# Kernel optimization log

Measured on AMD Instinct MI355X. Metric: run time of the kernel, lower is better.

## Reference

```python
import jax, jax.numpy as jnp
import numpy as np

D_MODEL = 1024
N_HEADS = 16
D_K = D_MODEL // N_HEADS
D_FF = 4096
B, S = 4, 2048
EPS = 1e-5


def setup_inputs() -> dict:
    key = jax.random.key(0)
    ks = jax.random.split(key, 16)
    s = 0.02
    inp = {
        'x': jax.random.normal(ks[0], (B, S, D_MODEL), dtype=jnp.float32),
        'Wq': jax.random.normal(ks[1], (D_MODEL, D_MODEL), dtype=jnp.float32) * s,
        'bq': jnp.zeros((D_MODEL,), jnp.float32),
        'Wk': jax.random.normal(ks[2], (D_MODEL, D_MODEL), dtype=jnp.float32) * s,
        'bk': jnp.zeros((D_MODEL,), jnp.float32),
        'Wv': jax.random.normal(ks[3], (D_MODEL, D_MODEL), dtype=jnp.float32) * s,
        'bv': jnp.zeros((D_MODEL,), jnp.float32),
        'Wo': jax.random.normal(ks[4], (D_MODEL, D_MODEL), dtype=jnp.float32) * s,
        'bo': jnp.zeros((D_MODEL,), jnp.float32),
        'W1': jax.random.normal(ks[5], (D_MODEL, D_FF), dtype=jnp.float32) * s,
        'b1': jnp.zeros((D_FF,), jnp.float32),
        'W2': jax.random.normal(ks[6], (D_FF, D_MODEL), dtype=jnp.float32) * s,
        'b2': jnp.zeros((D_MODEL,), jnp.float32),
        'g1': jnp.ones((D_MODEL,), jnp.float32),
        'be1': jnp.zeros((D_MODEL,), jnp.float32),
        'g2': jnp.ones((D_MODEL,), jnp.float32),
        'be2': jnp.zeros((D_MODEL,), jnp.float32),
    }
    return inp


def _layernorm(x, g, b):
    mu = jnp.mean(x, axis=-1, keepdims=True)
    var = jnp.var(x, axis=-1, keepdims=True)
    return (x - mu) * jax.lax.rsqrt(var + EPS) * g + b


def reference(x, Wq, bq, Wk, bk, Wv, bv, Wo, bo, W1, b1, W2, b2, g1, be1, g2, be2):
    # Multi-head self-attention (mask=None, dropout in eval -> identity)
    q = (x @ Wq + bq).reshape(B, S, N_HEADS, D_K).transpose(0, 2, 1, 3)  # [B,H,S,Dk]
    k = (x @ Wk + bk).reshape(B, S, N_HEADS, D_K).transpose(0, 2, 1, 3)
    v = (x @ Wv + bv).reshape(B, S, N_HEADS, D_K).transpose(0, 2, 1, 3)
    scores = jnp.einsum('bhqd,bhkd->bhqk', q, k) / jnp.sqrt(jnp.float32(D_K))
    attn = jax.nn.softmax(scores, axis=-1)
    out = jnp.einsum('bhqk,bhkd->bhqd', attn, v)          # [B,H,S,Dk]
    out = out.transpose(0, 2, 1, 3).reshape(B, S, D_MODEL)
    att_out = out @ Wo + bo
    x2 = _layernorm(x + att_out, g1, be1)
    ff = jax.nn.relu(x2 @ W1 + b1) @ W2 + b2
    return _layernorm(x2 + ff, g2, be2)
```

## Files before the change

kernel.cpp:

```cpp
#include <hip/hip_runtime.h>
#include <hip/hip_bf16.h>

typedef __attribute__((ext_vector_type(8)))  __bf16 bf16x8;
typedef __attribute__((ext_vector_type(4)))  float  f32x4;
typedef __attribute__((ext_vector_type(16))) float  f32x16;

static __device__ __forceinline__ unsigned short f2bf(float x) {
    unsigned int u = __float_as_uint(x);
    unsigned int r = (u + 0x7FFFu + ((u >> 16) & 1u)) >> 16;
    return (unsigned short)r;
}
static __device__ __forceinline__ float bf2f(unsigned short u) {
    return __uint_as_float(((unsigned int)u) << 16);
}

static __device__ __forceinline__ float fast_exp2(float x) {
    float r;
    asm volatile("v_exp_f32 %0, %1\n\ts_nop 1" : "=v"(r) : "v"(x));
    return r;
}
static __device__ __forceinline__ unsigned int cvt_pk_bf16(float a, float b) {
    unsigned int r;
    asm("v_cvt_pk_bf16_f32 %0, %1, %2" : "=v"(r) : "v"(a), "v"(b));
    return r;
}

static __device__ __forceinline__ void gload_lds16(const ushort* g, ushort* l) {
    __builtin_amdgcn_global_load_lds((const __attribute__((address_space(1))) void*)g,
                                     (__attribute__((address_space(3))) void*)l, 16, 0, 0);
}

static __device__ __forceinline__ int xcd_swz(int id, int nwg) {
    return (id & 7) * (nwg >> 3) + (id >> 3);
}

__global__ __launch_bounds__(256) void cast_bf16_kernel(const float* __restrict__ in,
                                                        ushort* __restrict__ out, int n4) {
    int i = blockIdx.x * 256 + threadIdx.x;
    if (i < n4) {
        float4 v = reinterpret_cast<const float4*>(in)[i];
        ushort4 o;
        o.x = f2bf(v.x); o.y = f2bf(v.y); o.z = f2bf(v.z); o.w = f2bf(v.w);
        reinterpret_cast<ushort4*>(out)[i] = o;
    }
}

__global__ __launch_bounds__(256) void transpose_cast_kernel(const float* __restrict__ in,
                                                             ushort* __restrict__ out,
                                                             int K, int N) {
    __shared__ float tile[32][33];
    const int tx = threadIdx.x;
    const int ty = threadIdx.y;
    const int n0 = blockIdx.x * 32;
    const int k0 = blockIdx.y * 32;
    for (int i = ty; i < 32; i += 8)
        tile[i][tx] = in[(size_t)(k0 + i) * N + n0 + tx];
    __syncthreads();
    for (int i = ty; i < 32; i += 8)
        out[(size_t)(n0 + i) * K + k0 + tx] = f2bf(tile[tx][i]);
}

template<int RELU, int OUTBF>
__global__ __launch_bounds__(256) void gemm_bt(const ushort* __restrict__ A,
                                               const ushort* __restrict__ Bt,
                                               const float* __restrict__ bias,
                                               void* __restrict__ Cp,
                                               int M, int N, int K) {
    __shared__ ushort As[128 * 32];
    __shared__ ushort Bs[128 * 32];
    const int tid  = threadIdx.x;
    const int lane = tid & 63;
    const int w    = tid >> 6;
    const int wr   = w >> 1, wc = w & 1;
    const int nwg = gridDim.x * gridDim.y;
    int wid = xcd_swz(blockIdx.y * gridDim.x + blockIdx.x, nwg);
    const int bx = wid % gridDim.x;
    const int by = wid / gridDim.x;
    const int m0 = by * 128;
    const int n0 = bx * 128;
    const int lr = lane & 15;
    const int lk = (lane >> 4) * 8;

    const int r0 = w * 32 + (lane >> 2);
    const int c8 = (lane & 3) * 8;
    const ushort* gA0 = A  + (size_t)(m0 + r0)      * K + c8;
    const ushort* gA1 = A  + (size_t)(m0 + r0 + 16) * K + c8;
    const ushort* gB0 = Bt + (size_t)(n0 + r0)      * K + c8;
    const ushort* gB1 = Bt + (size_t)(n0 + r0 + 16) * K + c8;
    ushort* lA0 = &As[w * 1024];
    ushort* lA1 = &As[w * 1024 + 512];
    ushort* lB0 = &Bs[w * 1024];
    ushort* lB1 = &Bs[w * 1024 + 512];

    f32x4 acc[4][4];
    const f32x4 z = {0.f, 0.f, 0.f, 0.f};
    for (int i = 0; i < 4; i++) for (int j = 0; j < 4; j++) acc[i][j] = z;

    for (int k0 = 0; k0 < K; k0 += 32) {
        __syncthreads();
        gload_lds16(gA0 + k0, lA0);
        gload_lds16(gA1 + k0, lA1);
        gload_lds16(gB0 + k0, lB0);
        gload_lds16(gB1 + k0, lB1);
        __syncthreads();

        bf16x8 af[4], bfr[4];
        for (int i = 0; i < 4; i++)
            af[i] = *reinterpret_cast<const bf16x8*>(&As[(wr * 64 + i * 16 + lr) * 32 + lk]);
        for (int j = 0; j < 4; j++)
            bfr[j] = *reinterpret_cast<const bf16x8*>(&Bs[(wc * 64 + j * 16 + lr) * 32 + lk]);
        for (int i = 0; i < 4; i++)
            for (int j = 0; j < 4; j++)
                acc[i][j] = __builtin_amdgcn_mfma_f32_16x16x32_bf16(af[i], bfr[j], acc[i][j], 0, 0, 0);
    }

    const int rbase = (lane >> 4) * 4;
    for (int i = 0; i < 4; i++) {
        for (int j = 0; j < 4; j++) {
            const int col = n0 + wc * 64 + j * 16 + lr;
            const float bv = bias[col];
            for (int r = 0; r < 4; r++) {
                const int row = m0 + wr * 64 + i * 16 + rbase + r;
                float v = acc[i][j][r] + bv;
                if (RELU) v = v > 0.f ? v : 0.f;
                if (OUTBF) ((ushort*)Cp)[(size_t)row * N + col] = f2bf(v);
                else       ((float*)Cp)[(size_t)row * N + col] = v;
            }
        }
    }
}

__global__ __launch_bounds__(256) void gemm_qkv(const ushort* __restrict__ A,
                                                const ushort* __restrict__ Bt,
                                                const float* __restrict__ bq,
                                                const float* __restrict__ bk,
                                                const float* __restrict__ bv,
                                                ushort* __restrict__ Cp) {
    const int K = 1024;
    __shared__ ushort As[128 * 32];
    __shared__ ushort Bs[128 * 32];
    const int tid  = threadIdx.x;
    const int lane = tid & 63;
    const int w    = tid >> 6;
    const int wr   = w >> 1, wc = w & 1;
    const int nwg = gridDim.x * gridDim.y;
    int wid = xcd_swz(blockIdx.y * gridDim.x + blockIdx.x, nwg);
    const int bx = wid % gridDim.x;
    const int by = wid / gridDim.x;
    const int m0 = by * 128;
    const int n0 = bx * 128;
    const int lr = lane & 15;
    const int lk = (lane >> 4) * 8;

    const int r0 = w * 32 + (lane >> 2);
    const int c8 = (lane & 3) * 8;
    const ushort* gA0 = A  + (size_t)(m0 + r0)      * K + c8;
    const ushort* gA1 = A  + (size_t)(m0 + r0 + 16) * K + c8;
    const ushort* gB0 = Bt + (size_t)(n0 + r0)      * K + c8;
    const ushort* gB1 = Bt + (size_t)(n0 + r0 + 16) * K + c8;
    ushort* lA0 = &As[w * 1024];
    ushort* lA1 = &As[w * 1024 + 512];
    ushort* lB0 = &Bs[w * 1024];
    ushort* lB1 = &Bs[w * 1024 + 512];

    f32x4 acc[4][4];
    const f32x4 z = {0.f, 0.f, 0.f, 0.f};
    for (int i = 0; i < 4; i++) for (int j = 0; j < 4; j++) acc[i][j] = z;

    for (int k0 = 0; k0 < K; k0 += 32) {
        __syncthreads();
        gload_lds16(gA0 + k0, lA0);
        gload_lds16(gA1 + k0, lA1);
        gload_lds16(gB0 + k0, lB0);
        gload_lds16(gB1 + k0, lB1);
        __syncthreads();

        bf16x8 af[4], bfr[4];
        for (int i = 0; i < 4; i++)
            af[i] = *reinterpret_cast<const bf16x8*>(&As[(wr * 64 + i * 16 + lr) * 32 + lk]);
        for (int j = 0; j < 4; j++)
            bfr[j] = *reinterpret_cast<const bf16x8*>(&Bs[(wc * 64 + j * 16 + lr) * 32 + lk]);
        for (int i = 0; i < 4; i++)
            for (int j = 0; j < 4; j++)
                acc[i][j] = __builtin_amdgcn_mfma_f32_16x16x32_bf16(af[i], bfr[j], acc[i][j], 0, 0, 0);
    }

    const float* bias = (n0 < 1024) ? bq : (n0 < 2048 ? bk : bv);
    const float qscale = (n0 < 1024) ? 0.18033688f : 1.0f;
    const int nb = n0 & 1023;
    const int rbase = (lane >> 4) * 4;
    for (int i = 0; i < 4; i++) {
        for (int j = 0; j < 4; j++) {
            const int cloc = wc * 64 + j * 16 + lr;
            const float bv_ = bias[nb + cloc];
            for (int r = 0; r < 4; r++) {
                const int row = m0 + wr * 64 + i * 16 + rbase + r;
                Cp[(size_t)row * 3072 + n0 + cloc] = f2bf((acc[i][j][r] + bv_) * qscale);
            }
        }
    }
}

#define ASWZ(row, col) ((row) * 64 + ((col) ^ ((((row) ^ ((row) >> 3)) & 7) << 3)))

__global__ __launch_bounds__(256, 3) void attn_kernel(const ushort* __restrict__ QKV,
                                                      ushort* __restrict__ O) {
    __shared__ ushort Ks[2][4096];
    __shared__ ushort Vt[2][4096];
    const int tid  = threadIdx.x;
    const int lane = tid & 63;
    const int w    = tid >> 6;
    const int l31  = lane & 31;
    const int hi   = lane >> 5;

    int blk = xcd_swz(blockIdx.x, gridDim.x);
    const int qb = blk & 15;
    const int h  = (blk >> 4) & 15;
    const int b  = blk >> 8;
    const int s0 = qb * 128 + w * 32;
    const size_t rowb   = (size_t)b * 2048;
    const size_t base_q = rowb * 3072 + (size_t)h * 64;
    const size_t base_k = base_q + 1024;
    const size_t base_v = base_q + 2048;
    const size_t base_o = rowb * 1024 + (size_t)h * 64;

    bf16x8 qf[4];
#pragma unroll
    for (int ks = 0; ks < 4; ks++)
        qf[ks] = *reinterpret_cast<const bf16x8*>(
            &QKV[base_q + (size_t)(s0 + l31) * 3072 + ks * 16 + 8 * hi]);

    int off8[2][4];
#pragma unroll
    for (int sub = 0; sub < 2; sub++)
#pragma unroll
        for (int ks = 0; ks < 4; ks++)
            off8[sub][ks] = ASWZ(sub * 32 + l31, ks * 16 + 8 * hi);

    const int tS  = tid >> 3;
    const int ccS = tid & 7;
    int vwoff[2][8];
#pragma unroll
    for (int i = 0; i < 2; i++)
#pragma unroll
        for (int jj = 0; jj < 8; jj++)
            vwoff[i][jj] = ASWZ(ccS * 8 + jj, tS + i * 32);
    const int t1  = tS + 32;
    const int sz0 = (tS ^ (tS >> 3)) & 7;
    const int sz1 = (t1 ^ (t1 >> 3)) & 7;
    const ushort* pK0 = QKV + base_k + (size_t)tS * 3072 + (ccS ^ sz0) * 8;
    const ushort* pK1 = QKV + base_k + (size_t)t1 * 3072 + (ccS ^ sz1) * 8;
    const ushort* pV0 = QKV + base_v + (size_t)tS * 3072 + ccS * 8;
    const ushort* pV1 = QKV + base_v + (size_t)t1 * 3072 + ccS * 8;
    const size_t step = (size_t)64 * 3072;

    gload_lds16(pK0, &Ks[0][w * 512]);
    gload_lds16(pK1, &Ks[0][2048 + w * 512]);
    {
        int4 v0 = *reinterpret_cast<const int4*>(pV0);
        int4 v1 = *reinterpret_cast<const int4*>(pV1);
        const ushort* vs0 = reinterpret_cast<const ushort*>(&v0);
        const ushort* vs1 = reinterpret_cast<const ushort*>(&v1);
#pragma unroll
        for (int jj = 0; jj < 8; jj++) Vt[0][vwoff[0][jj]] = vs0[jj];
#pragma unroll
        for (int jj = 0; jj < 8; jj++) Vt[0][vwoff[1][jj]] = vs1[jj];
    }
    pK0 += step; pK1 += step; pV0 += step; pV1 += step;
    __syncthreads();

    f32x16 oacc0, oacc1;
    for (int i = 0; i < 16; i++) { oacc0[i] = 0.f; oacc1[i] = 0.f; }
    float lacc = 0.f;
    int cur = 0;

    for (int it = 0; it < 32; ++it) {
        int4 nv0, nv1;
        if (it < 31) {
            gload_lds16(pK0, &Ks[cur ^ 1][w * 512]);
            gload_lds16(pK1, &Ks[cur ^ 1][2048 + w * 512]);
            nv0 = *reinterpret_cast<const int4*>(pV0);
            nv1 = *reinterpret_cast<const int4*>(pV1);
            pK0 += step; pK1 += step; pV0 += step; pV1 += step;
        }

        f32x16 sa0, sa1;
        for (int i = 0; i < 16; i++) { sa0[i] = 0.f; sa1[i] = 0.f; }
        __builtin_amdgcn_s_setprio(1);
#pragma unroll
        for (int ks = 0; ks < 4; ks++) {
            bf16x8 k0 = *reinterpret_cast<const bf16x8*>(&Ks[cur][off8[0][ks]]);
            sa0 = __builtin_amdgcn_mfma_f32_32x32x16_bf16(k0, qf[ks], sa0, 0, 0, 0);
        }
#pragma unroll
        for (int ks = 0; ks < 4; ks++) {
            bf16x8 k1 = *reinterpret_cast<const bf16x8*>(&Ks[cur][off8[1][ks]]);
            sa1 = __builtin_amdgcn_mfma_f32_32x32x16_bf16(k1, qf[ks], sa1, 0, 0, 0);
        }
        __builtin_amdgcn_s_setprio(0);

        unsigned pk0[8], pk1[8];
#pragma unroll
        for (int i = 0; i < 8; i++) {
            float plo = fast_exp2(sa0[2 * i]);
            float phi = fast_exp2(sa0[2 * i + 1]);
            lacc += plo + phi;
            pk0[i] = cvt_pk_bf16(plo, phi);
        }
#pragma unroll
        for (int i = 0; i < 8; i++) {
            float plo = fast_exp2(sa1[2 * i]);
            float phi = fast_exp2(sa1[2 * i + 1]);
            lacc += plo + phi;
            pk1[i] = cvt_pk_bf16(plo, phi);
        }

        __builtin_amdgcn_s_setprio(1);
#pragma unroll
        for (int ks = 0; ks < 4; ks++) {
            const int bi = 4 * (ks & 1);
            unsigned a, bb, c, d;
            if (ks < 2) { a = pk0[bi]; bb = pk0[bi + 1]; c = pk0[bi + 2]; d = pk0[bi + 3]; }
            else        { a = pk1[bi]; bb = pk1[bi + 1]; c = pk1[bi + 2]; d = pk1[bi + 3]; }
            asm("v_permlane32_swap_b32 %0, %1" : "+v"(a), "+v"(c));
            asm("v_permlane32_swap_b32 %0, %1" : "+v"(bb), "+v"(d));
            union { unsigned u[4]; bf16x8 v; } fr;
            fr.u[0] = a; fr.u[1] = bb; fr.u[2] = c; fr.u[3] = d;
            bf16x8 v0 = *reinterpret_cast<const bf16x8*>(&Vt[cur][off8[0][ks]]);
            oacc0 = __builtin_amdgcn_mfma_f32_32x32x16_bf16(fr.v, v0, oacc0, 0, 0, 0);
            bf16x8 v1 = *reinterpret_cast<const bf16x8*>(&Vt[cur][off8[1][ks]]);
            oacc1 = __builtin_amdgcn_mfma_f32_32x32x16_bf16(fr.v, v1, oacc1, 0, 0, 0);
        }
        __builtin_amdgcn_s_setprio(0);

        if (it < 31) {
            const ushort* vs0 = reinterpret_cast<const ushort*>(&nv0);
            const ushort* vs1 = reinterpret_cast<const ushort*>(&nv1);
#pragma unroll
            for (int jj = 0; jj < 8; jj++) Vt[cur ^ 1][vwoff[0][jj]] = vs0[jj];
#pragma unroll
            for (int jj = 0; jj < 8; jj++) Vt[cur ^ 1][vwoff[1][jj]] = vs1[jj];
        }
        __syncthreads();
        cur ^= 1;
    }

    const float ltot = lacc + __shfl_xor(lacc, 32);
    const float inv  = 1.f / ltot;

#pragma unroll
    for (int r = 0; r < 16; r++) {
        const int qloc = (r & 3) + 8 * (r >> 2) + 4 * hi;
        const float invq = __shfl(inv, qloc);
        const size_t rowoff = base_o + (size_t)(s0 + qloc) * 1024 + l31;
        O[rowoff]      = f2bf(oacc0[r] * invq);
        O[rowoff + 32] = f2bf(oacc1[r] * invq);
    }
}

__global__ __launch_bounds__(256) void ln_res_fb(const float* __restrict__ x,
                                                 const ushort* __restrict__ y,
                                                 const float* __restrict__ g,
                                                 const float* __restrict__ be,
                                                 ushort* __restrict__ outb) {
    const int row = blockIdx.x;
    const int tid = threadIdx.x;
    const float4 xv = reinterpret_cast<const float4*>(x + (size_t)row * 1024)[tid];
    const ushort4 yv = reinterpret_cast<const ushort4*>(y + (size_t)row * 1024)[tid];
    float v[4] = {xv.x + bf2f(yv.x), xv.y + bf2f(yv.y), xv.z + bf2f(yv.z), xv.w + bf2f(yv.w)};
    float s  = v[0] + v[1] + v[2] + v[3];
    float s2 = v[0]*v[0] + v[1]*v[1] + v[2]*v[2] + v[3]*v[3];
    for (int off = 32; off; off >>= 1) { s += __shfl_down(s, off); s2 += __shfl_down(s2, off); }
    __shared__ float red[8];
    const int w = tid >> 6, lane = tid & 63;
    if (lane == 0) { red[w] = s; red[4 + w] = s2; }
    __syncthreads();
    if (tid == 0) {
        const float ts  = red[0] + red[1] + red[2] + red[3];
        const float ts2 = red[4] + red[5] + red[6] + red[7];
        const float mu  = ts * (1.f / 1024.f);
        const float var = ts2 * (1.f / 1024.f) - mu * mu;
        red[0] = mu;
        red[1] = rsqrtf(var + 1e-5f);
    }
    __syncthreads();
    const float mu = red[0], rs = red[1];
    const float4 gv = reinterpret_cast<const float4*>(g)[tid];
    const float4 bv = reinterpret_cast<const float4*>(be)[tid];
    ushort4 ob;
    ob.x = f2bf((v[0] - mu) * rs * gv.x + bv.x);
    ob.y = f2bf((v[1] - mu) * rs * gv.y + bv.y);
    ob.z = f2bf((v[2] - mu) * rs * gv.z + bv.z);
    ob.w = f2bf((v[3] - mu) * rs * gv.w + bv.w);
    reinterpret_cast<ushort4*>(outb + (size_t)row * 1024)[tid] = ob;
}

__global__ __launch_bounds__(256) void ln_res_bb(const ushort* __restrict__ x,
                                                 const ushort* __restrict__ y,
                                                 const float* __restrict__ g,
                                                 const float* __restrict__ be,
                                                 float* __restrict__ outf) {
    const int row = blockIdx.x;
    const int tid = threadIdx.x;
    const ushort4 xv = reinterpret_cast<const ushort4*>(x + (size_t)row * 1024)[tid];
    const ushort4 yv = reinterpret_cast<const ushort4*>(y + (size_t)row * 1024)[tid];
    float v[4] = {bf2f(xv.x) + bf2f(yv.x), bf2f(xv.y) + bf2f(yv.y),
                  bf2f(xv.z) + bf2f(yv.z), bf2f(xv.w) + bf2f(yv.w)};
    float s  = v[0] + v[1] + v[2] + v[3];
    float s2 = v[0]*v[0] + v[1]*v[1] + v[2]*v[2] + v[3]*v[3];
    for (int off = 32; off; off >>= 1) { s += __shfl_down(s, off); s2 += __shfl_down(s2, off); }
    __shared__ float red[8];
    const int w = tid >> 6, lane = tid & 63;
    if (lane == 0) { red[w] = s; red[4 + w] = s2; }
    __syncthreads();
    if (tid == 0) {
        const float ts  = red[0] + red[1] + red[2] + red[3];
        const float ts2 = red[4] + red[5] + red[6] + red[7];
        const float mu  = ts * (1.f / 1024.f);
        const float var = ts2 * (1.f / 1024.f) - mu * mu;
        red[0] = mu;
        red[1] = rsqrtf(var + 1e-5f);
    }
    __syncthreads();
    const float mu = red[0], rs = red[1];
    const float4 gv = reinterpret_cast<const float4*>(g)[tid];
    const float4 bv = reinterpret_cast<const float4*>(be)[tid];
    float4 of;
    of.x = (v[0] - mu) * rs * gv.x + bv.x;
    of.y = (v[1] - mu) * rs * gv.y + bv.y;
    of.z = (v[2] - mu) * rs * gv.z + bv.z;
    of.w = (v[3] - mu) * rs * gv.w + bv.w;
    reinterpret_cast<float4*>(outf + (size_t)row * 1024)[tid] = of;
}

extern "C" void kernel_launch(void* const* d_in, const int* in_sizes, int n_in,
                              void* d_out, int out_size, void* d_ws, size_t ws_size,
                              hipStream_t stream) {
    const float* x  = (const float*)d_in[0];
    const float* Wq = (const float*)d_in[1];  const float* bq = (const float*)d_in[2];
    const float* Wk = (const float*)d_in[3];  const float* bk = (const float*)d_in[4];
    const float* Wv = (const float*)d_in[5];  const float* bv = (const float*)d_in[6];
    const float* Wo = (const float*)d_in[7];  const float* bo = (const float*)d_in[8];
    const float* W1 = (const float*)d_in[9];  const float* b1 = (const float*)d_in[10];
    const float* W2 = (const float*)d_in[11]; const float* b2 = (const float*)d_in[12];
    const float* g1 = (const float*)d_in[13]; const float* be1 = (const float*)d_in[14];
    const float* g2 = (const float*)d_in[15]; const float* be2 = (const float*)d_in[16];

    char* ws = (char*)d_ws;
    const size_t MBy = (size_t)1 << 20;
    ushort* xb    = (ushort*)(ws + 0 * MBy);
    ushort* wqkvT = (ushort*)(ws + 16 * MBy);
    ushort* woT   = (ushort*)(ws + 22 * MBy);
    ushort* w1T   = (ushort*)(ws + 24 * MBy);
    ushort* w2T   = (ushort*)(ws + 32 * MBy);
    ushort* QKVb  = (ushort*)(ws + 40 * MBy);
    ushort* AOb   = (ushort*)(ws + 88 * MBy);
    ushort* h1    = (ushort*)(ws + 40 * MBy);
    ushort* y1b   = (ushort*)(ws + 104 * MBy);
    ushort* y2b   = (ushort*)(ws + 104 * MBy);
    ushort* x2b   = (ushort*)(ws + 120 * MBy);
    (void)ws_size; (void)n_in; (void)in_sizes; (void)out_size;

    const int M = 8192;

    cast_bf16_kernel<<<(M * 1024 / 4 + 255) / 256, 256, 0, stream>>>(x, xb, M * 1024 / 4);
    dim3 tb(32, 8);
    transpose_cast_kernel<<<dim3(32, 32),  tb, 0, stream>>>(Wq, wqkvT,               1024, 1024);
    transpose_cast_kernel<<<dim3(32, 32),  tb, 0, stream>>>(Wk, wqkvT + 1024 * 1024, 1024, 1024);
    transpose_cast_kernel<<<dim3(32, 32),  tb, 0, stream>>>(Wv, wqkvT + 2048 * 1024, 1024, 1024);
    transpose_cast_kernel<<<dim3(32, 32),  tb, 0, stream>>>(Wo, woT, 1024, 1024);
    transpose_cast_kernel<<<dim3(128, 32), tb, 0, stream>>>(W1, w1T, 1024, 4096);
    transpose_cast_kernel<<<dim3(32, 128), tb, 0, stream>>>(W2, w2T, 4096, 1024);

    gemm_qkv<<<dim3(24, 64), 256, 0, stream>>>(xb, wqkvT, bq, bk, bv, QKVb);

    attn_kernel<<<1024, 256, 0, stream>>>(QKVb, AOb);

    gemm_bt<0, 1><<<dim3(8, 64), 256, 0, stream>>>(AOb, woT, bo, y1b, M, 1024, 1024);

    ln_res_fb<<<M, 256, 0, stream>>>(x, y1b, g1, be1, x2b);

    gemm_bt<1, 1><<<dim3(32, 64), 256, 0, stream>>>(x2b, w1T, b1, h1, M, 4096, 1024);
    gemm_bt<0, 1><<<dim3(8, 64), 256, 0, stream>>>(h1, w2T, b2, y2b, M, 1024, 4096);

    ln_res_bb<<<M, 256, 0, stream>>>(x2b, y2b, g2, be2, (float*)d_out);
}
```

Measured before the change: 450.8 us.

## Replace GEMMs with 4-stage pipelined 256x128-tile kernel using async LDS loads

```diff
diff --git a/kernel.cpp b/kernel.cpp
--- a/kernel.cpp
+++ b/kernel.cpp
@@ -28,6 +28,12 @@
 static __device__ __forceinline__ void gload_lds16(const ushort* g, ushort* l) {
     __builtin_amdgcn_global_load_lds((const __attribute__((address_space(1))) void*)g,
                                      (__attribute__((address_space(3))) void*)l, 16, 0, 0);
+}
+
+static __device__ __forceinline__ void barrier_fence() {
+    __builtin_amdgcn_s_barrier();
+    __builtin_amdgcn_sched_barrier(0);
+    asm volatile("" ::: "memory");
 }
 
 static __device__ __forceinline__ int xcd_swz(int id, int nwg) {
@@ -60,142 +66,114 @@
         out[(size_t)(n0 + i) * K + k0 + tx] = f2bf(tile[tx][i]);
 }
 
-template<int RELU, int OUTBF>
-__global__ __launch_bounds__(256) void gemm_bt(const ushort* __restrict__ A,
-                                               const ushort* __restrict__ Bt,
-                                               const float* __restrict__ bias,
-                                               void* __restrict__ Cp,
-                                               int M, int N, int K) {
-    __shared__ ushort As[128 * 32];
-    __shared__ ushort Bs[128 * 32];
+template<int RELU, int OUTBF, int QKV>
+__global__ __launch_bounds__(512, 2) void gemm_deep(const ushort* __restrict__ A,
+                                                    const ushort* __restrict__ Bt,
+                                                    const float* __restrict__ b0,
+                                                    const float* __restrict__ b1_,
+                                                    const float* __restrict__ b2_,
+                                                    void* __restrict__ Cp,
+                                                    int M, int N, int K) {
+    __shared__ ushort As[4 * 8192];
+    __shared__ ushort Bs[4 * 4096];
     const int tid  = threadIdx.x;
     const int lane = tid & 63;
     const int w    = tid >> 6;
-    const int wr   = w >> 1, wc = w & 1;
-    const int nwg = gridDim.x * gridDim.y;
+    const int wr   = w >> 1;
+    const int wc   = w & 1;
+    const int nwg  = gridDim.x * gridDim.y;
     int wid = xcd_swz(blockIdx.y * gridDim.x + blockIdx.x, nwg);
     const int bx = wid % gridDim.x;
     const int by = wid / gridDim.x;
-    const int m0 = by * 128;
+    const int m0 = by * 256;
     const int n0 = bx * 128;
     const int lr = lane & 15;
     const int lk = (lane >> 4) * 8;
 
-    const int r0 = w * 32 + (lane >> 2);
-    const int c8 = (lane & 3) * 8;
-    const ushort* gA0 = A  + (size_t)(m0 + r0)      * K + c8;
-    const ushort* gA1 = A  + (size_t)(m0 + r0 + 16) * K + c8;
-    const ushort* gB0 = Bt + (size_t)(n0 + r0)      * K + c8;
-    const ushort* gB1 = Bt + (size_t)(n0 + r0 + 16) * K + c8;
-    ushort* lA0 = &As[w * 1024];
-    ushort* lA1 = &As[w * 1024 + 512];
-    ushort* lB0 = &Bs[w * 1024];
-    ushort* lB1 = &Bs[w * 1024 + 512];
+    const int r0 = tid >> 2;
+    const int c8 = (tid & 3) * 8;
+    const ushort* gA0 = A  + (size_t)(m0 + r0)       * K + c8;
+    const ushort* gA1 = A  + (size_t)(m0 + 128 + r0) * K + c8;
+    const ushort* gB  = Bt + (size_t)(n0 + r0)       * K + c8;
+    const int wbase = w * 512;
 
     f32x4 acc[4][4];
     const f32x4 z = {0.f, 0.f, 0.f, 0.f};
-    for (int i = 0; i < 4; i++) for (int j = 0; j < 4; j++) acc[i][j] = z;
-
-    for (int k0 = 0; k0 < K; k0 += 32) {
-        __syncthreads();
-        gload_lds16(gA0 + k0, lA0);
-        gload_lds16(gA1 + k0, lA1);
-        gload_lds16(gB0 + k0, lB0);
-        gload_lds16(gB1 + k0, lB1);
-        __syncthreads();
-
+#pragma unroll
+    for (int i = 0; i < 4; i++)
+#pragma unroll
+        for (int j = 0; j < 4; j++) acc[i][j] = z;
+
+    const int nt = K >> 5;
+
+#pragma unroll
+    for (int t = 0; t < 3; ++t) {
+        const int kn = t * 32;
+        gload_lds16(gA0 + kn, &As[t * 8192 + wbase]);
+        gload_lds16(gA1 + kn, &As[t * 8192 + 4096 + wbase]);
+        gload_lds16(gB  + kn, &Bs[t * 4096 + wbase]);
+    }
+
+    for (int t = 0; t < nt; ++t) {
+        const int ahead = nt - 1 - t;
+        if (ahead >= 3) {
+            const int kn = (t + 3) * 32;
+            const int bn = (t + 3) & 3;
+            gload_lds16(gA0 + kn, &As[bn * 8192 + wbase]);
+            gload_lds16(gA1 + kn, &As[bn * 8192 + 4096 + wbase]);
+            gload_lds16(gB  + kn, &Bs[bn * 4096 + wbase]);
+            asm volatile("s_waitcnt vmcnt(9)" ::: "memory");
+        } else if (ahead == 2) {
+            asm volatile("s_waitcnt vmcnt(6)" ::: "memory");
+        } else if (ahead == 1) {
+            asm volatile("s_waitcnt vmcnt(3)" ::: "memory");
+        } else {
+            asm volatile("s_waitcnt vmcnt(0)" ::: "memory");
+        }
+        barrier_fence();
+
+        const ushort* Asb = &As[(t & 3) * 8192];
+        const ushort* Bsb = &Bs[(t & 3) * 4096];
         bf16x8 af[4], bfr[4];
+#pragma unroll
         for (int i = 0; i < 4; i++)
-            af[i] = *reinterpret_cast<const bf16x8*>(&As[(wr * 64 + i * 16 + lr) * 32 + lk]);
+            af[i] = *reinterpret_cast<const bf16x8*>(&Asb[(wr * 64 + i * 16 + lr) * 32 + lk]);
+#pragma unroll
         for (int j = 0; j < 4; j++)
-            bfr[j] = *reinterpret_cast<const bf16x8*>(&Bs[(wc * 64 + j * 16 + lr) * 32 + lk]);
+            bfr[j] = *reinterpret_cast<const bf16x8*>(&Bsb[(wc * 64 + j * 16 + lr) * 32 + lk]);
+#pragma unroll
         for (int i = 0; i < 4; i++)
+#pragma unroll
             for (int j = 0; j < 4; j++)
                 acc[i][j] = __builtin_amdgcn_mfma_f32_16x16x32_bf16(af[i], bfr[j], acc[i][j], 0, 0, 0);
-    }
-
+
+        barrier_fence();
+    }
+
+    const float* bias;
+    float qscale = 1.0f;
+    if (QKV) {
+        bias = (n0 < 1024) ? b0 : (n0 < 2048 ? b1_ : b2_);
+        if (n0 < 1024) qscale = 0.18033688f;
+    } else {
+        bias = b0;
+    }
+    const int nb = QKV ? (n0 & 1023) : n0;
     const int rbase = (lane >> 4) * 4;
+#pragma unroll
     for (int i = 0; i < 4; i++) {
+#pragma unroll
         for (int j = 0; j < 4; j++) {
-            const int col = n0 + wc * 64 + j * 16 + lr;
-            const float bv = bias[col];
+            const int cloc = wc * 64 + j * 16 + lr;
+            const float bv = bias[nb + cloc];
+#pragma unroll
             for (int r = 0; r < 4; r++) {
                 const int row = m0 + wr * 64 + i * 16 + rbase + r;
                 float v = acc[i][j][r] + bv;
                 if (RELU) v = v > 0.f ? v : 0.f;
-                if (OUTBF) ((ushort*)Cp)[(size_t)row * N + col] = f2bf(v);
-                else       ((float*)Cp)[(size_t)row * N + col] = v;
-            }
-        }
-    }
-}
-
-__global__ __launch_bounds__(256) void gemm_qkv(const ushort* __restrict__ A,
-                                                const ushort* __restrict__ Bt,
-                                                const float* __restrict__ bq,
-                                                const float* __restrict__ bk,
-                                                const float* __restrict__ bv,
-                                                ushort* __restrict__ Cp) {
-    const int K = 1024;
-    __shared__ ushort As[128 * 32];
-    __shared__ ushort Bs[128 * 32];
-    const int tid  = threadIdx.x;
-    const int lane = tid & 63;
-    const int w    = tid >> 6;
-    const int wr   = w >> 1, wc = w & 1;
-    const int nwg = gridDim.x * gridDim.y;
-    int wid = xcd_swz(blockIdx.y * gridDim.x + blockIdx.x, nwg);
-    const int bx = wid % gridDim.x;
-    const int by = wid / gridDim.x;
-    const int m0 = by * 128;
-    const int n0 = bx * 128;
-    const int lr = lane & 15;
-    const int lk = (lane >> 4) * 8;
-
-    const int r0 = w * 32 + (lane >> 2);
-    const int c8 = (lane & 3) * 8;
-    const ushort* gA0 = A  + (size_t)(m0 + r0)      * K + c8;
-    const ushort* gA1 = A  + (size_t)(m0 + r0 + 16) * K + c8;
-    const ushort* gB0 = Bt + (size_t)(n0 + r0)      * K + c8;
-    const ushort* gB1 = Bt + (size_t)(n0 + r0 + 16) * K + c8;
-    ushort* lA0 = &As[w * 1024];
-    ushort* lA1 = &As[w * 1024 + 512];
-    ushort* lB0 = &Bs[w * 1024];
-    ushort* lB1 = &Bs[w * 1024 + 512];
-
-    f32x4 acc[4][4];
-    const f32x4 z = {0.f, 0.f, 0.f, 0.f};
-    for (int i = 0; i < 4; i++) for (int j = 0; j < 4; j++) acc[i][j] = z;
-
-    for (int k0 = 0; k0 < K; k0 += 32) {
-        __syncthreads();
-        gload_lds16(gA0 + k0, lA0);
-        gload_lds16(gA1 + k0, lA1);
-        gload_lds16(gB0 + k0, lB0);
-        gload_lds16(gB1 + k0, lB1);
-        __syncthreads();
-
-        bf16x8 af[4], bfr[4];
-        for (int i = 0; i < 4; i++)
-            af[i] = *reinterpret_cast<const bf16x8*>(&As[(wr * 64 + i * 16 + lr) * 32 + lk]);
-        for (int j = 0; j < 4; j++)
-            bfr[j] = *reinterpret_cast<const bf16x8*>(&Bs[(wc * 64 + j * 16 + lr) * 32 + lk]);
-        for (int i = 0; i < 4; i++)
-            for (int j = 0; j < 4; j++)
-                acc[i][j] = __builtin_amdgcn_mfma_f32_16x16x32_bf16(af[i], bfr[j], acc[i][j], 0, 0, 0);
-    }
-
-    const float* bias = (n0 < 1024) ? bq : (n0 < 2048 ? bk : bv);
-    const float qscale = (n0 < 1024) ? 0.18033688f : 1.0f;
-    const int nb = n0 & 1023;
-    const int rbase = (lane >> 4) * 4;
-    for (int i = 0; i < 4; i++) {
-        for (int j = 0; j < 4; j++) {
-            const int cloc = wc * 64 + j * 16 + lr;
-            const float bv_ = bias[nb + cloc];
-            for (int r = 0; r < 4; r++) {
-                const int row = m0 + wr * 64 + i * 16 + rbase + r;
-                Cp[(size_t)row * 3072 + n0 + cloc] = f2bf((acc[i][j][r] + bv_) * qscale);
+                if (QKV)  v *= qscale;
+                if (OUTBF) ((ushort*)Cp)[(size_t)row * N + n0 + cloc] = f2bf(v);
+                else       ((float*)Cp)[(size_t)row * N + n0 + cloc] = v;
             }
         }
     }
@@ -347,7 +325,6 @@
 
     const float ltot = lacc + __shfl_xor(lacc, 32);
     const float inv  = 1.f / ltot;
-
 #pragma unroll
     for (int r = 0; r < 16; r++) {
         const int qloc = (r & 3) + 8 * (r >> 2) + 4 * hi;
@@ -472,16 +449,20 @@
     transpose_cast_kernel<<<dim3(128, 32), tb, 0, stream>>>(W1, w1T, 1024, 4096);
     transpose_cast_kernel<<<dim3(32, 128), tb, 0, stream>>>(W2, w2T, 4096, 1024);
 
-    gemm_qkv<<<dim3(24, 64), 256, 0, stream>>>(xb, wqkvT, bq, bk, bv, QKVb);
+    gemm_deep<0, 1, 1><<<dim3(24, 32), 512, 0, stream>>>(xb, wqkvT, bq, bk, bv, QKVb,
+                                                         M, 3072, 1024);
 
     attn_kernel<<<1024, 256, 0, stream>>>(QKVb, AOb);
 
-    gemm_bt<0, 1><<<dim3(8, 64), 256, 0, stream>>>(AOb, woT, bo, y1b, M, 1024, 1024);
+    gemm_deep<0, 1, 0><<<dim3(8, 32), 512, 0, stream>>>(AOb, woT, bo, nullptr, nullptr, y1b,
+                                                        M, 1024, 1024);
 
     ln_res_fb<<<M, 256, 0, stream>>>(x, y1b, g1, be1, x2b);
 
-    gemm_bt<1, 1><<<dim3(32, 64), 256, 0, stream>>>(x2b, w1T, b1, h1, M, 4096, 1024);
-    gemm_bt<0, 1><<<dim3(8, 64), 256, 0, stream>>>(h1, w2T, b2, y2b, M, 1024, 4096);
+    gemm_deep<1, 1, 0><<<dim3(32, 32), 512, 0, stream>>>(x2b, w1T, b1, nullptr, nullptr, h1,
+                                                         M, 4096, 1024);
+    gemm_deep<0, 1, 0><<<dim3(8, 32), 512, 0, stream>>>(h1, w2T, b2, nullptr, nullptr, y2b,
+                                                        M, 1024, 4096);
 
     ln_res_bb<<<M, 256, 0, stream>>>(x2b, y2b, g2, be2, (float*)d_out);
 }
```

Measured after the change: 502.8 us. 1.12x slower.
